# Optimization experiments

Hardware: AMD Instinct MI355X
Metric: run time of the kernel (lower is better)

## Reference

```python
import jax, jax.numpy as jnp
import numpy as np

B, LQ, LKV, LT, C, H = 4, 1024, 1344, 320, 768, 12
DH = C // H
SCALE = DH ** -0.5
HID = 4 * C
EPS = 1e-5


def _ln(x, g, b):
    m = jnp.mean(x, axis=-1, keepdims=True)
    v = jnp.mean((x - m) ** 2, axis=-1, keepdims=True)
    return (x - m) * jax.lax.rsqrt(v + EPS) * g + b


def setup_inputs() -> dict:
    key = jax.random.key(0)
    ks = jax.random.split(key, 16)
    s = lambda k, shape, sc=0.02: jax.random.normal(k, shape, dtype=jnp.float32) * sc
    return {
        "tem_mask": s(ks[0], (B, LT, C), 1.0),
        "q": s(ks[1], (B, LQ, C), 1.0),
        "kv": s(ks[2], (B, LKV, C), 1.0),
        "attn_pos": s(ks[3], (1, H, LQ, LKV), 1.0),
        "ln1q_g": jnp.ones((C,)), "ln1q_b": jnp.zeros((C,)),
        "ln1kv_g": jnp.ones((C,)), "ln1kv_b": jnp.zeros((C,)),
        "Wq": s(ks[4], (C, C)), "bq": jnp.zeros((C,)),
        "Wkv": s(ks[5], (C, 2 * C)), "bkv": jnp.zeros((2 * C,)),
        "Wp": s(ks[6], (C, C)), "bp": jnp.zeros((C,)),
        "ln2_g": jnp.ones((C,)), "ln2_b": jnp.zeros((C,)),
        "W1": s(ks[7], (C, HID)), "b1": jnp.zeros((HID,)),
        "W2": s(ks[8], (HID, C)), "b2": jnp.zeros((C,)),
    }


def reference(tem_mask, q, kv, attn_pos, ln1q_g, ln1q_b, ln1kv_g, ln1kv_b,
              Wq, bq, Wkv, bkv, Wp, bp, ln2_g, ln2_b, W1, b1, W2, b2):
    qn = _ln(q, ln1q_g, ln1q_b)
    kvn = _ln(kv, ln1kv_g, ln1kv_b)
    # projections (attn_pos_encoding_only branch)
    qh = (qn @ Wq + bq).reshape(B, LQ, H, DH).transpose(0, 2, 1, 3)  # (B,H,Lq,Dh)
    kvp = kvn @ Wkv + bkv
    k, v = kvp[:, :, :C], kvp[:, :, C:]
    v = v.at[:, :LT, :].add(tem_mask)  # add template mask to template tokens
    kh = k.reshape(B, LKV, H, DH).transpose(0, 2, 1, 3)
    vh = v.reshape(B, LKV, H, DH).transpose(0, 2, 1, 3)
    attn = jnp.einsum('bhqd,bhkd->bhqk', qh, kh) * SCALE + attn_pos
    attn = jax.nn.softmax(attn, axis=-1)
    x = jnp.einsum('bhqk,bhkd->bhqd', attn, vh)
    x = x.transpose(0, 2, 1, 3).reshape(B, LQ, C)
    x = x @ Wp + bp
    q = q + x  # residual 1 (drop_path = Identity, dropout eval)
    h = _ln(q, ln2_g, ln2_b)
    h = jax.nn.gelu(h @ W1 + b1, approximate=False)
    h = h @ W2 + b2
    return q + h
```

## Files before the change

kernel.cpp:

```cpp
#include <hip/hip_runtime.h>
#include <hip/hip_bf16.h>
#include <math.h>

typedef __bf16 bf16x8 __attribute__((ext_vector_type(8)));
typedef float f32x4 __attribute__((ext_vector_type(4)));

__device__ __forceinline__ __hip_bfloat16 f2bf(float v){ return __float2bfloat16(v); }

__device__ __forceinline__ void gload16(const void* g, void* l){
  __builtin_amdgcn_global_load_lds(
      (const __attribute__((address_space(1))) void*)g,
      (__attribute__((address_space(3))) void*)l, 16, 0, 0);
}

__global__ void transpose_all(const float* __restrict__ Wq, const float* __restrict__ Wkv,
                              const float* __restrict__ Wp, const float* __restrict__ W1,
                              const float* __restrict__ W2,
                              __hip_bfloat16* __restrict__ oq, __hip_bfloat16* __restrict__ okv,
                              __hip_bfloat16* __restrict__ op_, __hip_bfloat16* __restrict__ o1,
                              __hip_bfloat16* __restrict__ o2){
  __shared__ float tile[32][33];
  const int bid = blockIdx.x;
  const float* in; __hip_bfloat16* out; int K, N, local;
  if(bid < 576)        { in=Wq;  out=oq;  K=768;  N=768;  local=bid; }
  else if(bid < 1728)  { in=Wkv; out=okv; K=768;  N=1536; local=bid-576; }
  else if(bid < 2304)  { in=Wp;  out=op_; K=768;  N=768;  local=bid-1728; }
  else if(bid < 4608)  { in=W1;  out=o1;  K=768;  N=3072; local=bid-2304; }
  else                 { in=W2;  out=o2;  K=3072; N=768;  local=bid-4608; }
  const int nbx = N/32;
  const int n0 = (local % nbx)*32, k0 = (local / nbx)*32;
  int tx = threadIdx.x, ty = threadIdx.y;
#pragma unroll
  for(int i=0;i<4;i++) tile[ty+i*8][tx] = in[(size_t)(k0+ty+i*8)*N + n0+tx];
  __syncthreads();
#pragma unroll
  for(int i=0;i<4;i++) out[(size_t)(n0+ty+i*8)*K + k0+tx] = f2bf(tile[tx][ty+i*8]);
}

__global__ __launch_bounds__(256) void transpose_vt(const __hip_bfloat16* __restrict__ vbuf,
                                                    __hip_bfloat16* __restrict__ vt){
  __shared__ __hip_bfloat16 tl[64][72];
  const int bh = blockIdx.x;
  const int kt = blockIdx.y;
  const int b = bh / 12, h = bh % 12;
  const int tid = threadIdx.x;
  const int r = tid >> 3, c = (tid & 7) * 8;
#pragma unroll
  for(int j=0;j<2;j++){
    uint4 v = *(const uint4*)(vbuf + ((size_t)(b*1344 + kt*64 + r + j*32))*768 + h*64 + c);
    *(uint4*)&tl[r + j*32][c] = v;
  }
  __syncthreads();
#pragma unroll
  for(int j=0;j<2;j++){
    int d = r + j*32;
    __hip_bfloat16 tmp[8];
#pragma unroll
    for(int i=0;i<8;i++) tmp[i] = tl[c + i][d];
    *(uint4*)(vt + ((size_t)(bh*64 + d))*1344 + kt*64 + c) = *(const uint4*)tmp;
  }
}

__device__ __forceinline__ void ln_body(const float* rp, const float* g, const float* b,
                                        __hip_bfloat16* op, int t){
  float x0 = rp[t], x1 = rp[t+256], x2 = rp[t+512];
  float s = x0+x1+x2, ss = x0*x0+x1*x1+x2*x2;
#pragma unroll
  for(int o=32;o>0;o>>=1){ s += __shfl_down(s,o); ss += __shfl_down(ss,o); }
  __shared__ float red[10];
  if((t&63)==0){ red[t>>6]=s; red[4+(t>>6)]=ss; }
  __syncthreads();
  if(t==0){
    float S=red[0]+red[1]+red[2]+red[3], SS=red[4]+red[5]+red[6]+red[7];
    float m=S*(1.f/768.f);
    red[8]=m; red[9]=SS*(1.f/768.f)-m*m;
  }
  __syncthreads();
  float m=red[8], r=rsqrtf(red[9]+1e-5f);
  op[t]     = f2bf((x0-m)*r*g[t]     + b[t]);
  op[t+256] = f2bf((x1-m)*r*g[t+256] + b[t+256]);
  op[t+512] = f2bf((x2-m)*r*g[t+512] + b[t+512]);
}

__global__ __launch_bounds__(256) void ln_qkv(const float* __restrict__ q, const float* __restrict__ kv,
    const float* __restrict__ qg, const float* __restrict__ qb,
    const float* __restrict__ kg, const float* __restrict__ kb2,
    __hip_bfloat16* __restrict__ qn, __hip_bfloat16* __restrict__ kvn){
  int row = blockIdx.x, t = threadIdx.x;
  if(row < 4096) ln_body(q + (size_t)row*768, qg, qb, qn + (size_t)row*768, t);
  else { row -= 4096; ln_body(kv + (size_t)row*768, kg, kb2, kvn + (size_t)row*768, t); }
}

__global__ __launch_bounds__(256) void ln_kernel(const float* __restrict__ in,
    const float* __restrict__ g, const float* __restrict__ b,
    __hip_bfloat16* __restrict__ out){
  int row = blockIdx.x, t = threadIdx.x;
  ln_body(in + (size_t)row*768, g, b, out + (size_t)row*768, t);
}

template<int BM, int BN, int EPI>
__global__ __launch_bounds__(256) void gemm_gl(
    const __hip_bfloat16* __restrict__ A, const __hip_bfloat16* __restrict__ BT,
    const float* __restrict__ bias, int M, int N, int K,
    void* __restrict__ out, const void* __restrict__ aux0, void* __restrict__ out2){
  constexpr int WR = (BM==128 || BN==64) ? 2 : 1;
  constexpr int WC = 4/WR;
  constexpr int MF = BM/(WR*16);
  constexpr int NF = BN/(WC*16);
  __shared__ char sA[2][BM*128];
  __shared__ char sB[2][BN*128];
  const int tid = threadIdx.x;
  const int l = tid & 63, w = tid >> 6;
  const int lg = l >> 4, li = l & 15;
  const int wrow = (WR==2) ? (w>>1)*(BM/2) : 0;
  const int wcol = (WC==2) ? (w&1)*(BN/2) : w*(BN/4);
  const int bm = blockIdx.x * BM;
  const int bn = blockIdx.y * BN;
  const int arow = w*(BM/4) + (l>>3);
  const int brow = w*(BN/4) + (l>>3);
  const int scol = ((((l&7)*16) ^ ((l>>3)<<4)) >> 1);

  auto stage = [&](int buf, int kt){
    const int k0 = kt*64;
#pragma unroll
    for(int i=0;i<BM/32;i++)
      gload16(A  + (size_t)(bm+arow+i*8)*K + k0 + scol, sA[buf] + (w*(BM/4))*128 + i*1024);
#pragma unroll
    for(int i=0;i<BN/32;i++)
      gload16(BT + (size_t)(bn+brow+i*8)*K + k0 + scol, sB[buf] + (w*(BN/4))*128 + i*1024);
  };

  f32x4 acc[MF][NF] = {};
  const int nk = K >> 6;
  stage(0, 0);
  __syncthreads();
  for(int kt=0; kt<nk; ++kt){
    const int cur = kt & 1;
    if(kt+1 < nk) stage(cur^1, kt+1);
#pragma unroll
    for(int kk=0;kk<2;kk++){
      const int kb = kk*64 + lg*16;
      bf16x8 af[MF], bfr[NF];
#pragma unroll
      for(int m=0;m<MF;m++){
        int row = wrow+m*16+li;
        af[m] = *(const bf16x8*)(sA[cur] + row*128 + (kb ^ ((row&7)<<4)));
      }
#pragma unroll
      for(int n=0;n<NF;n++){
        int row = wcol+n*16+li;
        bfr[n] = *(const bf16x8*)(sB[cur] + row*128 + (kb ^ ((row&7)<<4)));
      }
#pragma unroll
      for(int m=0;m<MF;m++)
#pragma unroll
        for(int n=0;n<NF;n++)
          acc[m][n] = __builtin_amdgcn_mfma_f32_16x16x32_bf16(af[m], bfr[n], acc[m][n],0,0,0);
    }
    __syncthreads();
  }
#pragma unroll
  for(int m=0;m<MF;m++){
#pragma unroll
    for(int n=0;n<NF;n++){
#pragma unroll
      for(int r=0;r<4;r++){
        int row = bm + wrow + m*16 + lg*4 + r;
        int col = bn + wcol + n*16 + li;
        float v = acc[m][n][r] + bias[col];
        if constexpr(EPI==0){
          ((__hip_bfloat16*)out)[(size_t)row*N + col] = f2bf(v * 0.125f);
        } else if constexpr(EPI==1){
          if(col < 768){
            ((__hip_bfloat16*)out)[(size_t)row*768 + col] = f2bf(v);
          } else {
            int c = col - 768;
            int bb = row / 1344, ii = row % 1344;
            if(ii < 320) v += ((const float*)aux0)[((size_t)bb*320 + ii)*768 + c];
            ((__hip_bfloat16*)out2)[(size_t)row*768 + c] = f2bf(v);
          }
        } else if constexpr(EPI==2){
          v += ((const float*)aux0)[(size_t)row*N + col];
          ((float*)out)[(size_t)row*N + col] = v;
        } else if constexpr(EPI==3){
          float gl = 0.5f * v * (1.0f + erff(v * 0.70710678118654752f));
          ((__hip_bfloat16*)out)[(size_t)row*N + col] = f2bf(gl);
        } else {
          v += ((const float*)aux0)[(size_t)row*N + col];
          ((float*)out)[(size_t)row*N + col] = v;
        }
      }
    }
  }
}

__global__ __launch_bounds__(256) void attn_kernel(
    const __hip_bfloat16* __restrict__ qh,
    const __hip_bfloat16* __restrict__ kb,
    const __hip_bfloat16* __restrict__ vt,
    const float* __restrict__ pos,
    __hip_bfloat16* __restrict__ xo){
  __shared__ char sK[2][8192];
  __shared__ char sV[2][8192];
  __shared__ char sP[4][2048];
  const int bid = blockIdx.x;
  const int qt = bid & 15, h = (bid >> 4) % 12, b = bid / 192;
  const int q0 = qt * 64;
  const int tid = threadIdx.x;
  const int l = tid & 63, w = tid >> 6;
  const int lg = l >> 4, li = l & 15;

  const int srow = w*16 + (l>>3);
  const int soff = (((l&7)*16) ^ ((l>>3)<<4)) >> 1;
  const __hip_bfloat16* ksrc = kb + ((size_t)b*1344 + srow)*768 + h*64 + soff;
  const __hip_bfloat16* vsrc = vt + ((size_t)(b*12+h)*64 + srow)*1344 + soff;

  bf16x8 aq[2];
  {
    const char* qp = (const char*)(qh + ((size_t)(b*1024 + q0 + w*16 + li))*768 + h*64);
    aq[0] = *(const bf16x8*)(qp + lg*16);
    aq[1] = *(const bf16x8*)(qp + 64 + lg*16);
  }
  const size_t posbase = ((size_t)h*1024 + q0 + w*16 + lg*4)*1344 + li;

  f32x4 accO[4] = {};
  float mrun[4], lrun[4];
#pragma unroll
  for(int r=0;r<4;r++){ mrun[r] = -1e30f; lrun[r] = 0.f; }

  auto stage = [&](int buf, int t){
    const size_t ko = (size_t)t*64*768;
    const size_t vo = (size_t)t*64;
    gload16(ksrc + ko,          sK[buf] + w*2048);
    gload16(ksrc + ko + 8*768,  sK[buf] + w*2048 + 1024);
    gload16(vsrc + vo,          sV[buf] + w*2048);
    gload16(vsrc + vo + 8*1344, sV[buf] + w*2048 + 1024);
  };
  auto ldpos = [&](int t, float pr[4][4]){
    const float* pp = pos + posbase + (size_t)t*64;
#pragma unroll
    for(int n=0;n<4;n++)
#pragma unroll
      for(int r=0;r<4;r++)
        pr[n][r] = __builtin_nontemporal_load(pp + (size_t)r*1344 + n*16);
  };

  float posr[4][4];
  ldpos(0, posr);
  stage(0, 0);
  __syncthreads();

  char* sPw = sP[w];
  for(int t=0; t<21; ++t){
    const int cur = t & 1;
    f32x4 accS[4] = {};
#pragma unroll
    for(int kk=0; kk<2; ++kk){
      const int kbyte = kk*64 + lg*16;
#pragma unroll
      for(int n=0;n<4;n++){
        int row = n*16 + li;
        bf16x8 bkf = *(const bf16x8*)(sK[cur] + row*128 + (kbyte ^ ((row&7)<<4)));
        accS[n] = __builtin_amdgcn_mfma_f32_16x16x32_bf16(aq[kk], bkf, accS[n], 0,0,0);
      }
    }
    if(t < 20) stage(cur^1, t+1);
    float npos[4][4];
    if(t < 20) ldpos(t+1, npos);

    float p[4][4], mt[4];
#pragma unroll
    for(int r=0;r<4;r++) mt[r] = -1e30f;
#pragma unroll
    for(int n=0;n<4;n++)
#pragma unroll
      for(int r=0;r<4;r++){
        float s = accS[n][r] + posr[n][r];
        p[n][r] = s;
        mt[r] = fmaxf(mt[r], s);
      }
#pragma unroll
    for(int r=0;r<4;r++){
#pragma unroll
      for(int o=1;o<16;o<<=1) mt[r] = fmaxf(mt[r], __shfl_xor(mt[r], o));
      float mnew = fmaxf(mrun[r], mt[r]);
      float sf = __expf(mrun[r]-mnew);
      mrun[r] = mnew;
      lrun[r] *= sf;
#pragma unroll
      for(int n=0;n<4;n++) accO[n][r] *= sf;
      float rs = 0.f;
#pragma unroll
      for(int n=0;n<4;n++){ p[n][r] = __expf(p[n][r]-mnew); rs += p[n][r]; }
#pragma unroll
      for(int o=1;o<16;o<<=1) rs += __shfl_xor(rs, o);
      lrun[r] += rs;
    }
#pragma unroll
    for(int n=0;n<4;n++)
#pragma unroll
      for(int r=0;r<4;r++){
        int qi = lg*4 + r, kj = n*16 + li;
        *(__hip_bfloat16*)(sPw + qi*128 + ((kj*2) ^ ((qi&7)<<4))) = f2bf(p[n][r]);
      }
#pragma unroll
    for(int kk=0; kk<2; ++kk){
      const int kbyte = kk*64 + lg*16;
      bf16x8 pa = *(const bf16x8*)(sPw + li*128 + (kbyte ^ ((li&7)<<4)));
#pragma unroll
      for(int n=0;n<4;n++){
        int d = n*16 + li;
        bf16x8 bvf = *(const bf16x8*)(sV[cur] + d*128 + (kbyte ^ ((d&7)<<4)));
        accO[n] = __builtin_amdgcn_mfma_f32_16x16x32_bf16(pa, bvf, accO[n], 0,0,0);
      }
    }
    if(t < 20){
#pragma unroll
      for(int n=0;n<4;n++)
#pragma unroll
        for(int r=0;r<4;r++) posr[n][r] = npos[n][r];
    }
    __syncthreads();
  }
#pragma unroll
  for(int n=0;n<4;n++)
#pragma unroll
    for(int r=0;r<4;r++){
      int row = b*1024 + q0 + w*16 + lg*4 + r;
      int col = h*64 + n*16 + li;
      xo[(size_t)row*768 + col] = f2bf(accO[n][r] / lrun[r]);
    }
}

extern "C" void kernel_launch(void* const* d_in, const int* in_sizes, int n_in,
                              void* d_out, int out_size, void* d_ws, size_t ws_size,
                              hipStream_t stream){
  const float* tem   = (const float*)d_in[0];
  const float* qin   = (const float*)d_in[1];
  const float* kvin  = (const float*)d_in[2];
  const float* pos   = (const float*)d_in[3];
  const float* ln1qg = (const float*)d_in[4];
  const float* ln1qb = (const float*)d_in[5];
  const float* ln1kg = (const float*)d_in[6];
  const float* ln1kb = (const float*)d_in[7];
  const float* Wq    = (const float*)d_in[8];
  const float* bq    = (const float*)d_in[9];
  const float* Wkv   = (const float*)d_in[10];
  const float* bkv   = (const float*)d_in[11];
  const float* Wp    = (const float*)d_in[12];
  const float* bp    = (const float*)d_in[13];
  const float* ln2g  = (const float*)d_in[14];
  const float* ln2b  = (const float*)d_in[15];
  const float* W1    = (const float*)d_in[16];
  const float* b1    = (const float*)d_in[17];
  const float* W2    = (const float*)d_in[18];
  const float* b2    = (const float*)d_in[19];

  char* ws = (char*)d_ws; size_t off = 0;
  auto alloc = [&](size_t n){ char* p = ws + off; off = (off + n + 255) & ~(size_t)255; return p; };
  __hip_bfloat16* WqT  = (__hip_bfloat16*)alloc((size_t)768*768*2);
  __hip_bfloat16* WkvT = (__hip_bfloat16*)alloc((size_t)1536*768*2);
  __hip_bfloat16* WpT  = (__hip_bfloat16*)alloc((size_t)768*768*2);
  __hip_bfloat16* W1T  = (__hip_bfloat16*)alloc((size_t)3072*768*2);
  __hip_bfloat16* W2T  = (__hip_bfloat16*)alloc((size_t)768*3072*2);
  __hip_bfloat16* qn   = (__hip_bfloat16*)alloc((size_t)4096*768*2);
  char* poolBase = alloc((size_t)5376*768*2*3 + (size_t)4096*768*2);
  __hip_bfloat16* kvn  = (__hip_bfloat16*)poolBase;
  __hip_bfloat16* kbuf = kvn  + (size_t)5376*768;
  __hip_bfloat16* vbuf = kbuf + (size_t)5376*768;
  __hip_bfloat16* qhb  = vbuf + (size_t)5376*768;
  __hip_bfloat16* xat  = (__hip_bfloat16*)alloc((size_t)4096*768*2);
  float*          x1f  = (float*)alloc((size_t)4096*768*4);
  __hip_bfloat16* vt   = kvn;
  __hip_bfloat16* hln  = qn;
  __hip_bfloat16* h1   = kvn;

  transpose_all<<<6912, dim3(32,8), 0, stream>>>(Wq, Wkv, Wp, W1, W2, WqT, WkvT, WpT, W1T, W2T);
  ln_qkv<<<4096+5376, 256, 0, stream>>>(qin, kvin, ln1qg, ln1qb, ln1kg, ln1kb, qn, kvn);

  gemm_gl<64,64,0>  <<<dim3(64, 12), 256, 0, stream>>>(qn,  WqT,  bq,  4096, 768,  768,  qhb, nullptr, nullptr);
  gemm_gl<128,128,1><<<dim3(42, 12), 256, 0, stream>>>(kvn, WkvT, bkv, 5376, 1536, 768,  kbuf, tem, vbuf);
  transpose_vt<<<dim3(48, 21), 256, 0, stream>>>(vbuf, vt);

  attn_kernel<<<768, 256, 0, stream>>>(qhb, kbuf, vt, pos, xat);

  gemm_gl<64,64,2>  <<<dim3(64, 12), 256, 0, stream>>>(xat, WpT,  bp,  4096, 768,  768,  x1f, qin, nullptr);
  ln_kernel<<<4096, 256, 0, stream>>>(x1f, ln2g, ln2b, hln);
  gemm_gl<128,128,3><<<dim3(32, 24), 256, 0, stream>>>(hln, W1T,  b1,  4096, 3072, 768,  h1, nullptr, nullptr);
  gemm_gl<64,64,4>  <<<dim3(64, 12), 256, 0, stream>>>(h1,  W2T,  b2,  4096, 768,  3072, (float*)d_out, x1f, nullptr);
}
```

Measured before the change: 248.9 us.

## Pipeline attention loop with ping-pong pos registers, lazy rescale, tanh GELU

Splits the attention loop into a two-step unrolled body that alternates between two positional-bias register sets, so the per-iteration register copy goes away. The end-of-iteration __syncthreads is replaced by a partial vmcnt wait plus a raw barrier, and s_setprio is raised around the MFMA blocks. Online-softmax rescaling of the running max, sum and output accumulator is now skipped unless the tile max grows by more than 8. The exact erf GELU in the FFN epilogue is replaced by a tanh approximation built from __expf, which changes numerics slightly.

```diff
diff --git a/kernel.cpp b/kernel.cpp
--- a/kernel.cpp
+++ b/kernel.cpp
@@ -183,8 +183,11 @@
           v += ((const float*)aux0)[(size_t)row*N + col];
           ((float*)out)[(size_t)row*N + col] = v;
         } else if constexpr(EPI==3){
-          float gl = 0.5f * v * (1.0f + erff(v * 0.70710678118654752f));
-          ((__hip_bfloat16*)out)[(size_t)row*N + col] = f2bf(gl);
+          float u = v*(0.7978845608f + 0.0356774081f*v*v);
+          float e = __expf(-2.f*fabsf(u));
+          float th = (1.f - e)/(1.f + e);
+          th = (u < 0.f) ? -th : th;
+          ((__hip_bfloat16*)out)[(size_t)row*N + col] = f2bf(0.5f*v*(1.f+th));
         } else {
           v += ((const float*)aux0)[(size_t)row*N + col];
           ((float*)out)[(size_t)row*N + col] = v;
@@ -236,7 +239,7 @@
     gload16(vsrc + vo,          sV[buf] + w*2048);
     gload16(vsrc + vo + 8*1344, sV[buf] + w*2048 + 1024);
   };
-  auto ldpos = [&](int t, float pr[4][4]){
+  auto ldpos = [&](int t, float (&pr)[4][4]){
     const float* pp = pos + posbase + (size_t)t*64;
 #pragma unroll
     for(int n=0;n<4;n++)
@@ -245,15 +248,18 @@
         pr[n][r] = __builtin_nontemporal_load(pp + (size_t)r*1344 + n*16);
   };
 
-  float posr[4][4];
-  ldpos(0, posr);
+  float pA[4][4], pB[4][4];
+  ldpos(0, pA);
   stage(0, 0);
   __syncthreads();
 
   char* sPw = sP[w];
-  for(int t=0; t<21; ++t){
+
+  auto body = [&](int t, float (&posr)[4][4], float (&npos)[4][4]){
     const int cur = t & 1;
+    const bool more = (t < 20);
     f32x4 accS[4] = {};
+    __builtin_amdgcn_s_setprio(1);
 #pragma unroll
     for(int kk=0; kk<2; ++kk){
       const int kbyte = kk*64 + lg*16;
@@ -264,9 +270,10 @@
         accS[n] = __builtin_amdgcn_mfma_f32_16x16x32_bf16(aq[kk], bkf, accS[n], 0,0,0);
       }
     }
-    if(t < 20) stage(cur^1, t+1);
-    float npos[4][4];
-    if(t < 20) ldpos(t+1, npos);
+    __builtin_amdgcn_s_setprio(0);
+    if(more) stage(cur^1, t+1);
+    asm volatile("" ::: "memory");
+    if(more) ldpos(t+1, npos);
 
     float p[4][4], mt[4];
 #pragma unroll
@@ -280,18 +287,28 @@
         mt[r] = fmaxf(mt[r], s);
       }
 #pragma unroll
+    for(int r=0;r<4;r++)
+#pragma unroll
+      for(int o=1;o<16;o<<=1) mt[r] = fmaxf(mt[r], __shfl_xor(mt[r], o));
+    bool need = false;
+#pragma unroll
+    for(int r=0;r<4;r++) need |= (mt[r] > mrun[r] + 8.f);
+    if(__any(need)){
+#pragma unroll
+      for(int r=0;r<4;r++){
+        float mnew = fmaxf(mrun[r], mt[r]);
+        float sf = __expf(mrun[r]-mnew);
+        mrun[r] = mnew;
+        lrun[r] *= sf;
+#pragma unroll
+        for(int n=0;n<4;n++) accO[n][r] *= sf;
+      }
+    }
+#pragma unroll
     for(int r=0;r<4;r++){
-#pragma unroll
-      for(int o=1;o<16;o<<=1) mt[r] = fmaxf(mt[r], __shfl_xor(mt[r], o));
-      float mnew = fmaxf(mrun[r], mt[r]);
-      float sf = __expf(mrun[r]-mnew);
-      mrun[r] = mnew;
-      lrun[r] *= sf;
-#pragma unroll
-      for(int n=0;n<4;n++) accO[n][r] *= sf;
       float rs = 0.f;
 #pragma unroll
-      for(int n=0;n<4;n++){ p[n][r] = __expf(p[n][r]-mnew); rs += p[n][r]; }
+      for(int n=0;n<4;n++){ p[n][r] = __expf(p[n][r]-mrun[r]); rs += p[n][r]; }
 #pragma unroll
       for(int o=1;o<16;o<<=1) rs += __shfl_xor(rs, o);
       lrun[r] += rs;
@@ -303,6 +320,7 @@
         int qi = lg*4 + r, kj = n*16 + li;
         *(__hip_bfloat16*)(sPw + qi*128 + ((kj*2) ^ ((qi&7)<<4))) = f2bf(p[n][r]);
       }
+    __builtin_amdgcn_s_setprio(1);
 #pragma unroll
     for(int kk=0; kk<2; ++kk){
       const int kbyte = kk*64 + lg*16;
@@ -314,14 +332,19 @@
         accO[n] = __builtin_amdgcn_mfma_f32_16x16x32_bf16(pa, bvf, accO[n], 0,0,0);
       }
     }
-    if(t < 20){
-#pragma unroll
-      for(int n=0;n<4;n++)
-#pragma unroll
-        for(int r=0;r<4;r++) posr[n][r] = npos[n][r];
-    }
-    __syncthreads();
-  }
+    __builtin_amdgcn_s_setprio(0);
+    if(more){
+      asm volatile("s_waitcnt vmcnt(16)" ::: "memory");
+      __builtin_amdgcn_s_barrier();
+    }
+  };
+
+  for(int tt=0; tt<10; ++tt){
+    body(2*tt,   pA, pB);
+    body(2*tt+1, pB, pA);
+  }
+  body(20, pA, pB);
+
 #pragma unroll
   for(int n=0;n<4;n++)
 #pragma unroll
```

Measured after the change: 237.6 us. 4.5% less time.
